# Kernel optimization log

Hardware: AMD Instinct MI355X
Metric: run time of the kernel (lower is better)

## Reference

```python
import jax, jax.numpy as jnp
import numpy as np

B, S, D, H = 8, 4096, 256, 256
MEM_COUNT = 3
FEAT = 7 * D + 2


def setup_inputs() -> dict:
    key = jax.random.key(0)
    ks = jax.random.split(key, 12)
    u = lambda k, shp: jax.random.uniform(k, shp, jnp.float32, -0.05, 0.05)
    return {
        "c": jax.random.normal(ks[0], (B, S, D), jnp.float32),
        "q": jax.random.normal(ks[1], (B, 1, D), jnp.float32),
        "len_c": jax.random.randint(ks[2], (B,), 1, S + 1),
        "att_weight": u(ks[3], (D, D)),
        "w1": u(ks[4], (H, FEAT)),
        "b1": jnp.zeros((H,), jnp.float32),
        "w2": u(ks[5], (1, H)),
        "b2": jnp.zeros((1,), jnp.float32),
        "w_ih": u(ks[6], (3 * D, D)),
        "w_hh": u(ks[7], (3 * D, D)),
        "b_ih": jnp.zeros((3 * D,), jnp.float32),
        "b_hh": jnp.zeros((3 * D,), jnp.float32),
    }


def gru_cell(x, h, w_ih, w_hh, b_ih, b_hh):
    # PyTorch GRUCell math
    gi = x @ w_ih.T + b_ih
    gh = h @ w_hh.T + b_hh
    i_r, i_z, i_n = jnp.split(gi, 3, axis=-1)
    h_r, h_z, h_n = jnp.split(gh, 3, axis=-1)
    r = jax.nn.sigmoid(i_r + h_r)
    z = jax.nn.sigmoid(i_z + h_z)
    n = jnp.tanh(i_n + r * h_n)
    return (1.0 - z) * n + z * h


def reference(c, q, len_c, att_weight, w1, b1, w2, b2, w_ih, w_hh, b_ih, b_hh):
    Bv, Sv, Dv = c.shape
    mask = jnp.arange(Sv)[None, :] < len_c[:, None]  # [B,S] valid positions
    cw = c @ att_weight                              # [B,S,D], reused each hop
    dot_q = jnp.einsum("bsd,bod->bso", cw, q)        # [B,S,1]
    m = q                                            # [B,1,D]
    atts = []
    for _ in range(MEM_COUNT):
        dot_m = jnp.einsum("bsd,bod->bso", cw, m)
        mb = jnp.broadcast_to(m, c.shape)
        qb = jnp.broadcast_to(q, c.shape)
        feat = jnp.concatenate(
            [c, mb, qb, c * q, c * m, jnp.abs(c - q), jnp.abs(c - m), dot_q, dot_m],
            axis=2,
        )                                            # [B,S,7D+2]
        h = jnp.tanh(feat @ w1.T + b1)               # [B,S,H]
        scores = (h @ w2.T + b2)[..., 0]             # [B,S]
        scores = jnp.where(mask, scores, -jnp.inf)
        att = jax.nn.softmax(scores, axis=1)
        att = jnp.where(mask, att, 0.0)[..., None]   # padded positions -> 0
        atts.append(att)
        e = (c * att).sum(axis=1)                    # [B,D]
        h_new = gru_cell(e, m[:, 0, :], w_ih, w_hh, b_ih, b_hh)
        m = h_new[:, None, :]
    return m[:, 0, :], jnp.stack(atts)
```

## Files before the change

kernel.cpp:

```cpp
#include <hip/hip_runtime.h>
#include <hip/hip_bf16.h>
#include <math.h>
#include <stdint.h>

#define B 8
#define S 4096
#define D 256
#define H 256
#define FEAT 1794
#define R (B*S)
#define DH (D*H)
#define NCH 64

typedef __bf16 bf16_t;
typedef __bf16 bf16x8 __attribute__((ext_vector_type(8)));
typedef float f32x4 __attribute__((ext_vector_type(4)));

__device__ __forceinline__ float waveReduceSum(float v) {
  #pragma unroll
  for (int off = 32; off; off >>= 1) v += __shfl_xor(v, off, 64);
  return v;
}

__global__ void k_init(const float* __restrict__ c, const float* __restrict__ q,
                       const float* __restrict__ w1, const float* __restrict__ A,
                       const int* __restrict__ len_c,
                       bf16_t* __restrict__ CBF, bf16_t* __restrict__ WAQ,
                       bf16_t* __restrict__ WAM, float* __restrict__ vq,
                       float* __restrict__ m0) {
  const int PREC_BLKS = R*D/2048;
  const int W_BLKS = DH/256;
  const int blk = blockIdx.x;
  if (blk < PREC_BLKS) {
    const int row0 = blk * 8;
    const int b = row0 >> 12;
    if ((row0 & 4095) >= len_c[b]) return;
    int gid = blk * 256 + threadIdx.x;
    const float* cp = c + (size_t)gid*8;
    float cv[8];
    *(float4*)(cv)   = *(const float4*)(cp);
    *(float4*)(cv+4) = *(const float4*)(cp + 4);
    bf16x8 cb;
    #pragma unroll
    for (int i = 0; i < 8; i++) cb[i] = (bf16_t)cv[i];
    *(bf16x8*)(CBF + (size_t)gid*8) = cb;
  } else if (blk < PREC_BLKS + W_BLKS) {
    int idx = (blk - PREC_BLKS) * 256 + threadIdx.x;
    int h = idx >> 8, k = idx & 255;
    const float* w1h = w1 + (size_t)h * FEAT;
    WAQ[idx] = (bf16_t)w1h[5*D + k];
    WAM[idx] = (bf16_t)w1h[6*D + k];
  } else {
    const int blk2 = blk - PREC_BLKS - W_BLKS;
    const int b = blk2 >> 6;
    const int lane = threadIdx.x & 63, wave = threadIdx.x >> 6;
    const int t = (blk2 & 63)*4 + wave;
    const int l4 = lane * 4;
    float4 q4 = *(const float4*)(q + b*D + l4);
    float4 a4 = *(const float4*)(A + (size_t)t*D + l4);
    float s = a4.x*q4.x + a4.y*q4.y + a4.z*q4.z + a4.w*q4.w;
    s = waveReduceSum(s);
    if (lane == 0) vq[b*D + t] = s;
    if (threadIdx.x < 4) {
      const int tt = (blk2 & 63)*4 + threadIdx.x;
      m0[b*D + tt] = q[b*D + tt];
    }
  }
}


__global__ void k_pm2(const float* __restrict__ A, const float* __restrict__ w1,
                      const float* __restrict__ b1, const float* __restrict__ q,
                      const float* __restrict__ min_,
                      float* __restrict__ vm, float* __restrict__ hb) {
  const int blk = blockIdx.x;
  const int b = blk >> 6;
  const int lane = threadIdx.x & 63, wave = threadIdx.x >> 6;
  const int t = (blk & 63)*4 + wave;
  const int l4 = lane * 4;
  float4 m4 = *(const float4*)(min_ + b*D + l4);
  float4 q4 = *(const float4*)(q + b*D + l4);
  float4 a4 = *(const float4*)(A + (size_t)t*D + l4);
  const float* w1r = w1 + (size_t)t*FEAT;
  float2 wm0 = *(const float2*)(w1r + D + l4);
  float2 wm1 = *(const float2*)(w1r + D + l4 + 2);
  float2 wq0 = *(const float2*)(w1r + 2*D + l4);
  float2 wq1 = *(const float2*)(w1r + 2*D + l4 + 2);
  float sv = a4.x*m4.x + a4.y*m4.y + a4.z*m4.z + a4.w*m4.w;
  float sh = m4.x*wm0.x + m4.y*wm0.y + m4.z*wm1.x + m4.w*wm1.y
           + q4.x*wq0.x + q4.y*wq0.y + q4.z*wq1.x + q4.w*wq1.y;
  sv = waveReduceSum(sv);
  sh = waveReduceSum(sh);
  if (lane == 0) { vm[b*D + t] = sv; hb[b*H + t] = b1[t] + sh; }
}

__global__ void k_comb(const float* __restrict__ w1, const float* __restrict__ q,
                       const float* __restrict__ min_,
                       const float* __restrict__ vq, const float* __restrict__ vm,
                       bf16_t* __restrict__ WCB) {
  int idx = blockIdx.x * 256 + threadIdx.x;
  int b = idx >> 16;
  int h = (idx >> 8) & 255;
  int k = idx & 255;
  const float* w1h = w1 + (size_t)h * FEAT;
  float v = w1h[k] + q[b*D + k]*w1h[3*D + k] + min_[b*D + k]*w1h[4*D + k]
          + vq[b*D + k]*w1h[7*D] + vm[b*D + k]*w1h[7*D + 1];
  WCB[idx] = (bf16_t)v;
}

__global__ __launch_bounds__(512, 4) void k_score6(
    const bf16_t* __restrict__ CBF,
    const bf16_t* __restrict__ WCB, const bf16_t* __restrict__ WAQ,
    const bf16_t* __restrict__ WAM,
    const float* __restrict__ q, const float* __restrict__ min_,
    const int* __restrict__ len_c,
    const float* __restrict__ hb, const float* __restrict__ w2,
    const float* __restrict__ b2, float* __restrict__ scores) {
  __shared__ char smem[49152];
  __shared__ float qshf[256], mshf[256];
  __shared__ float red[8][64];
  const int t = threadIdx.x;
  const int lane = t & 63, wave = t >> 6;
  const int r0 = blockIdx.x * 64;
  const int b = r0 >> 12;
  if ((r0 & 4095) >= len_c[b]) return;
  const int lrow = lane & 15;
  const int lk = (lane >> 4) * 8;
  const int n0 = wave * 32;

  if (t < 256) { qshf[t] = q[b*D + t]; mshf[t] = min_[b*D + t]; }

  const int srow = t >> 3, sl = t & 7;
  const int sp = sl ^ (srow & 7);
  const int swbase = srow*128 + sp*16;
  const bf16_t* cgp = CBF + (size_t)(r0 + srow)*D + sl*8;

  const bf16_t* bptrC = WCB + (size_t)b*DH;
  const bf16_t* bptrQ = WAQ;
  const bf16_t* bptrM = WAM;

  f32x4 acc[4][2];
  #pragma unroll
  for (int mi = 0; mi < 4; mi++)
    #pragma unroll
    for (int ni = 0; ni < 2; ni++) acc[mi][ni] = (f32x4){0.f,0.f,0.f,0.f};

  bf16x8 breg[2][6];
  #define LOADB(ks) { \
    const int kelem = (ks)*32 + lk; \
    _Pragma("unroll") \
    for (int ni = 0; ni < 2; ni++) { \
      const size_t co = (size_t)(n0 + ni*16 + lrow) * D + kelem; \
      breg[(ks)&1][ni*3+0] = *(const bf16x8*)(bptrC + co); \
      breg[(ks)&1][ni*3+1] = *(const bf16x8*)(bptrQ + co); \
      breg[(ks)&1][ni*3+2] = *(const bf16x8*)(bptrM + co); \
    } }

  #define STAGESC(mc, cc, cr) { \
    const int kof = (mc)*128 + (cc)*64 + sl*8; \
    float qv_[8], mv_[8]; \
    *(float4*)(qv_)   = *(const float4*)(qshf + kof); \
    *(float4*)(qv_+4) = *(const float4*)(qshf + kof + 4); \
    *(float4*)(mv_)   = *(const float4*)(mshf + kof); \
    *(float4*)(mv_+4) = *(const float4*)(mshf + kof + 4); \
    bf16x8 aqv_, amv_; \
    _Pragma("unroll") \
    for (int i = 0; i < 8; i++) { \
      float cf_ = (float)(cr)[i]; \
      aqv_[i] = (bf16_t)fabsf(cf_ - qv_[i]); \
      amv_[i] = (bf16_t)fabsf(cf_ - mv_[i]); \
    } \
    char* lb_ = smem + (cc)*8192 + swbase; \
    *(bf16x8*)(lb_)         = (cr); \
    *(bf16x8*)(lb_ + 16384) = aqv_; \
    *(bf16x8*)(lb_ + 32768) = amv_; \
  }

  bf16x8 cA = *(const bf16x8*)(cgp);
  bf16x8 cB = *(const bf16x8*)(cgp + 64);
  LOADB(0);
  __syncthreads();
  STAGESC(0, 0, cA);
  STAGESC(0, 1, cB);
  cA = *(const bf16x8*)(cgp + 128);
  cB = *(const bf16x8*)(cgp + 192);
  __syncthreads();

  #pragma unroll
  for (int ks = 0; ks < 4; ks++) {
    LOADB(ks + 1);
    const int cc = ks >> 1, kk = ks & 1;
    const int p = ((kk << 2) + (lane >> 4)) ^ (lane & 7);
    const char* lb = smem + cc*8192;
    #pragma unroll
    for (int mi = 0; mi < 4; mi++) {
      const int ro = (mi*16 + lrow)*128 + p*16;
      bf16x8 ac = *(const bf16x8*)(lb + ro);
      bf16x8 aq = *(const bf16x8*)(lb + 16384 + ro);
      bf16x8 am = *(const bf16x8*)(lb + 32768 + ro);
      #pragma unroll
      for (int ni = 0; ni < 2; ni++) {
        acc[mi][ni] = __builtin_amdgcn_mfma_f32_16x16x32_bf16(ac, breg[ks&1][ni*3+0], acc[mi][ni], 0, 0, 0);
        acc[mi][ni] = __builtin_amdgcn_mfma_f32_16x16x32_bf16(aq, breg[ks&1][ni*3+1], acc[mi][ni], 0, 0, 0);
        acc[mi][ni] = __builtin_amdgcn_mfma_f32_16x16x32_bf16(am, breg[ks&1][ni*3+2], acc[mi][ni], 0, 0, 0);
      }
    }
  }
  __syncthreads();
  STAGESC(1, 0, cA);
  STAGESC(1, 1, cB);
  __syncthreads();

  #pragma unroll
  for (int ks = 4; ks < 8; ks++) {
    if (ks < 7) LOADB(ks + 1);
    const int cc = (ks >> 1) & 1, kk = ks & 1;
    const int p = ((kk << 2) + (lane >> 4)) ^ (lane & 7);
    const char* lb = smem + cc*8192;
    #pragma unroll
    for (int mi = 0; mi < 4; mi++) {
      const int ro = (mi*16 + lrow)*128 + p*16;
      bf16x8 ac = *(const bf16x8*)(lb + ro);
      bf16x8 aq = *(const bf16x8*)(lb + 16384 + ro);
      bf16x8 am = *(const bf16x8*)(lb + 32768 + ro);
      #pragma unroll
      for (int ni = 0; ni < 2; ni++) {
        acc[mi][ni] = __builtin_amdgcn_mfma_f32_16x16x32_bf16(ac, breg[ks&1][ni*3+0], acc[mi][ni], 0, 0, 0);
        acc[mi][ni] = __builtin_amdgcn_mfma_f32_16x16x32_bf16(aq, breg[ks&1][ni*3+1], acc[mi][ni], 0, 0, 0);
        acc[mi][ni] = __builtin_amdgcn_mfma_f32_16x16x32_bf16(am, breg[ks&1][ni*3+2], acc[mi][ni], 0, 0, 0);
      }
    }
  }

  float hbv[2], w2v[2];
  #pragma unroll
  for (int ni = 0; ni < 2; ni++) {
    const int col = n0 + ni*16 + lrow;
    hbv[ni] = hb[b*H + col];
    w2v[ni] = w2[col];
  }
  #pragma unroll
  for (int mi = 0; mi < 4; mi++) {
    #pragma unroll
    for (int j = 0; j < 4; j++) {
      float ps = 0.f;
      #pragma unroll
      for (int ni = 0; ni < 2; ni++) {
        float x = acc[mi][ni][j] + hbv[ni];
        float ex = __expf(2.f * x);
        float th = 1.f - 2.f * __builtin_amdgcn_rcpf(ex + 1.f);
        ps += th * w2v[ni];
      }
      ps += __shfl_xor(ps, 1, 64);
      ps += __shfl_xor(ps, 2, 64);
      ps += __shfl_xor(ps, 4, 64);
      ps += __shfl_xor(ps, 8, 64);
      if (lrow == 0) red[wave][mi*16 + (lane >> 4)*4 + j] = ps;
    }
  }
  __syncthreads();
  if (t < 64) {
    float s = red[0][t] + red[1][t] + red[2][t] + red[3][t]
            + red[4][t] + red[5][t] + red[6][t] + red[7][t] + b2[0];
    scores[r0 + t] = s;
  }
}

__global__ __launch_bounds__(1024) void k_soft(const float* __restrict__ scores,
                                               const int* __restrict__ len_c,
                                               float* __restrict__ att) {
  const int b = blockIdx.x, t = threadIdx.x;
  const int len = len_c[b];
  __shared__ float rbuf[16];
  const float* sc = scores + b*S;
  float mx = -1e30f;
  for (int s = t; s < len; s += 1024) mx = fmaxf(mx, sc[s]);
  #pragma unroll
  for (int off = 32; off; off >>= 1) mx = fmaxf(mx, __shfl_xor(mx, off, 64));
  if ((t & 63) == 0) rbuf[t >> 6] = mx;
  __syncthreads();
  mx = rbuf[0];
  #pragma unroll
  for (int i = 1; i < 16; i++) mx = fmaxf(mx, rbuf[i]);
  __syncthreads();
  float sum = 0.f;
  float* ab = att + b*S;
  for (int s = t; s < S; s += 1024) {
    if (s < len) { float e = __expf(sc[s] - mx); ab[s] = e; sum += e; }
    else ab[s] = 0.f;
  }
  sum = waveReduceSum(sum);
  if ((t & 63) == 0) rbuf[t >> 6] = sum;
  __syncthreads();
  sum = 0.f;
  #pragma unroll
  for (int i = 0; i < 16; i++) sum += rbuf[i];
  const float inv = 1.f / sum;
  for (int s = t; s < len; s += 1024) ab[s] *= inv;
}

__global__ __launch_bounds__(256) void k_epart3(
    const bf16_t* __restrict__ CBF, const float* __restrict__ att,
    const int* __restrict__ len_c, float* __restrict__ epart) {
  const int b = blockIdx.x >> 6, ch = blockIdx.x & 63;
  const int t = threadIdx.x;
  const int s0 = ch * 64;
  if (s0 >= len_c[b]) {
    epart[(ch*B + b)*D + t] = 0.f;
    return;
  }
  __shared__ float esh[64];
  __shared__ float racc[8][256];
  if (t < 64) esh[t] = att[b*S + s0 + t];
  __syncthreads();
  const int cg = t & 31, rg = t >> 5;
  float a8[8];
  #pragma unroll
  for (int i = 0; i < 8; i++) a8[i] = 0.f;
  #pragma unroll
  for (int j = 0; j < 8; j++) {
    const int srow = rg + j*8;
    const bf16x8 cv = *(const bf16x8*)(CBF + (size_t)(b*S + s0 + srow)*D + cg*8);
    const float a = esh[srow];
    #pragma unroll
    for (int i = 0; i < 8; i++) a8[i] += a * (float)cv[i];
  }
  *(float4*)(&racc[rg][cg*8])     = *(float4*)(a8);
  *(float4*)(&racc[rg][cg*8 + 4]) = *(float4*)(a8 + 4);
  __syncthreads();
  float s = 0.f;
  #pragma unroll
  for (int g = 0; g < 8; g++) s += racc[g][t];
  epart[(ch*B + b)*D + t] = s;
}

__global__ __launch_bounds__(256) void k_gru2(
    const float* __restrict__ wih, const float* __restrict__ whh,
    const float* __restrict__ bih, const float* __restrict__ bhh,
    const float* __restrict__ epart, const float* __restrict__ min_,
    float* __restrict__ mout, float* __restrict__ out, const int write_out) {
  const int blk = blockIdx.x;
  const int b = blk >> 4;
  const int t0 = (blk & 15) << 4;
  const int t = threadIdx.x;
  const int lane = t & 63, wave = t >> 6;
  __shared__ float es[D], ms[D];
  float e = 0.f;
  #pragma unroll
  for (int ch = 0; ch < NCH; ch++) e += epart[(ch*B + b)*D + t];
  es[t] = e;
  ms[t] = min_[b*D + t];
  __syncthreads();
  const int l4 = lane * 4;
  float4 e4 = *(const float4*)(es + l4);
  float4 m4 = *(const float4*)(ms + l4);
  #pragma unroll
  for (int tl = 0; tl < 4; tl++) {
    const int tt = t0 + wave*4 + tl;
    float g[6];
    #pragma unroll
    for (int gg = 0; gg < 3; gg++) {
      const int j = gg*D + tt;
      const float4 wi4 = *(const float4*)(wih + (size_t)j*D + l4);
      const float4 wh4 = *(const float4*)(whh + (size_t)j*D + l4);
      float gi = e4.x*wi4.x + e4.y*wi4.y + e4.z*wi4.z + e4.w*wi4.w;
      float gh = m4.x*wh4.x + m4.y*wh4.y + m4.z*wh4.z + m4.w*wh4.w;
      g[gg]   = waveReduceSum(gi);
      g[3+gg] = waveReduceSum(gh);
    }
    if (lane == 0) {
      const int j0 = tt, j1 = D + tt, j2 = 2*D + tt;
      float gir = g[0] + bih[j0], giz = g[1] + bih[j1], gin = g[2] + bih[j2];
      float ghr = g[3] + bhh[j0], ghz = g[4] + bhh[j1], ghn = g[5] + bhh[j2];
      float rr = 1.f / (1.f + __expf(-(gir + ghr)));
      float zz = 1.f / (1.f + __expf(-(giz + ghz)));
      float nn = tanhf(gin + rr * ghn);
      float mn = (1.f - zz)*nn + zz*ms[tt];
      mout[b*D + tt] = mn;
      if (write_out) out[b*D + tt] = mn;
    }
  }
}

extern "C" void kernel_launch(void* const* d_in, const int* in_sizes, int n_in,
                              void* d_out, int out_size, void* d_ws, size_t ws_size,
                              hipStream_t stream) {
  const float* c   = (const float*)d_in[0];
  const float* q   = (const float*)d_in[1];
  const int*   len = (const int*)d_in[2];
  const float* A   = (const float*)d_in[3];
  const float* w1  = (const float*)d_in[4];
  const float* b1  = (const float*)d_in[5];
  const float* w2  = (const float*)d_in[6];
  const float* b2  = (const float*)d_in[7];
  const float* wih = (const float*)d_in[8];
  const float* whh = (const float*)d_in[9];
  const float* bih = (const float*)d_in[10];
  const float* bhh = (const float*)d_in[11];
  float* out = (float*)d_out;

  bf16_t* WCB = (bf16_t*)d_ws;
  bf16_t* WAQ = WCB + (size_t)B*DH;
  bf16_t* WAM = WAQ + DH;
  bf16_t* CBF = WAM + DH;
  float* fb = (float*)(CBF + (size_t)R*D);
  float* vq    = fb;
  float* vm    = vq + B*D;
  float* hb    = vm + B*D;
  float* m0    = hb + B*H;
  float* m1    = m0 + B*D;
  float* epart = m1 + B*D;
  float* sc    = epart + (size_t)NCH*B*D;

  k_init<<<R*D/2048 + DH/256 + B*64, 256, 0, stream>>>(c, q, w1, A, len, CBF, WAQ, WAM, vq, m0);

  for (int it = 0; it < 3; ++it) {
    float* min_ = (it & 1) ? m1 : m0;
    float* mout = (it & 1) ? m0 : m1;
    k_pm2<<<B*64, 256, 0, stream>>>(A, w1, b1, q, min_, vm, hb);
    k_comb<<<B*DH/256, 256, 0, stream>>>(w1, q, min_, vq, vm, WCB);
    k_score6<<<R/64, 512, 0, stream>>>(CBF, WCB, WAQ, WAM, q, min_, len, hb, w2, b2, sc);
    float* att = out + B*D + (size_t)it*R;
    k_soft<<<B, 1024, 0, stream>>>(sc, len, att);
    k_epart3<<<B*NCH, 256, 0, stream>>>(CBF, att, len, epart);
    k_gru2<<<B*16, 256, 0, stream>>>(wih, whh, bih, bhh, epart, min_, mout, out, it == 2 ? 1 : 0);
  }
}
```

Baseline: 156.4 us.

## Fold softmax into score, epart and GRU kernels; compact score grid over valid rows

```diff
diff --git a/kernel.cpp b/kernel.cpp
--- a/kernel.cpp
+++ b/kernel.cpp
@@ -108,22 +108,31 @@
   WCB[idx] = (bf16_t)v;
 }
 
-__global__ __launch_bounds__(512, 4) void k_score6(
+__global__ __launch_bounds__(512, 4) void k_score7(
     const bf16_t* __restrict__ CBF,
     const bf16_t* __restrict__ WCB, const bf16_t* __restrict__ WAQ,
     const bf16_t* __restrict__ WAM,
     const float* __restrict__ q, const float* __restrict__ min_,
     const int* __restrict__ len_c,
     const float* __restrict__ hb, const float* __restrict__ w2,
-    const float* __restrict__ b2, float* __restrict__ scores) {
+    const float* __restrict__ b2, float* __restrict__ esc) {
+  int b = 0, r0l = -1, accb = 0;
+  const int flat = blockIdx.x;
+  #pragma unroll
+  for (int bb = 0; bb < 8; bb++) {
+    const int nb = (len_c[bb] + 63) >> 6;
+    if (r0l < 0 && flat < accb + nb) { b = bb; r0l = (flat - accb) << 6; }
+    accb += nb;
+  }
+  if (r0l < 0) return;
+  const int len = len_c[b];
+  const int rowg = b*S + r0l;
+
   __shared__ char smem[49152];
   __shared__ float qshf[256], mshf[256];
   __shared__ float red[8][64];
   const int t = threadIdx.x;
   const int lane = t & 63, wave = t >> 6;
-  const int r0 = blockIdx.x * 64;
-  const int b = r0 >> 12;
-  if ((r0 & 4095) >= len_c[b]) return;
   const int lrow = lane & 15;
   const int lk = (lane >> 4) * 8;
   const int n0 = wave * 32;
@@ -133,7 +142,7 @@
   const int srow = t >> 3, sl = t & 7;
   const int sp = sl ^ (srow & 7);
   const int swbase = srow*128 + sp*16;
-  const bf16_t* cgp = CBF + (size_t)(r0 + srow)*D + sl*8;
+  const bf16_t* cgp = CBF + (size_t)(rowg + srow)*D + sl*8;
 
   const bf16_t* bptrC = WCB + (size_t)b*DH;
   const bf16_t* bptrQ = WAQ;
@@ -262,57 +271,30 @@
   if (t < 64) {
     float s = red[0][t] + red[1][t] + red[2][t] + red[3][t]
             + red[4][t] + red[5][t] + red[6][t] + red[7][t] + b2[0];
-    scores[r0 + t] = s;
-  }
-}
-
-__global__ __launch_bounds__(1024) void k_soft(const float* __restrict__ scores,
-                                               const int* __restrict__ len_c,
-                                               float* __restrict__ att) {
-  const int b = blockIdx.x, t = threadIdx.x;
-  const int len = len_c[b];
-  __shared__ float rbuf[16];
-  const float* sc = scores + b*S;
-  float mx = -1e30f;
-  for (int s = t; s < len; s += 1024) mx = fmaxf(mx, sc[s]);
-  #pragma unroll
-  for (int off = 32; off; off >>= 1) mx = fmaxf(mx, __shfl_xor(mx, off, 64));
-  if ((t & 63) == 0) rbuf[t >> 6] = mx;
-  __syncthreads();
-  mx = rbuf[0];
-  #pragma unroll
-  for (int i = 1; i < 16; i++) mx = fmaxf(mx, rbuf[i]);
-  __syncthreads();
-  float sum = 0.f;
-  float* ab = att + b*S;
-  for (int s = t; s < S; s += 1024) {
-    if (s < len) { float e = __expf(sc[s] - mx); ab[s] = e; sum += e; }
-    else ab[s] = 0.f;
-  }
-  sum = waveReduceSum(sum);
-  if ((t & 63) == 0) rbuf[t >> 6] = sum;
-  __syncthreads();
-  sum = 0.f;
-  #pragma unroll
-  for (int i = 0; i < 16; i++) sum += rbuf[i];
-  const float inv = 1.f / sum;
-  for (int s = t; s < len; s += 1024) ab[s] *= inv;
-}
-
-__global__ __launch_bounds__(256) void k_epart3(
-    const bf16_t* __restrict__ CBF, const float* __restrict__ att,
-    const int* __restrict__ len_c, float* __restrict__ epart) {
+    esc[b*S + r0l + t] = (r0l + t < len) ? __expf(s) : 0.f;
+  }
+}
+
+__global__ __launch_bounds__(256) void k_epart4(
+    const bf16_t* __restrict__ CBF, const float* __restrict__ esc,
+    const int* __restrict__ len_c, float* __restrict__ epart,
+    float* __restrict__ ssum) {
   const int b = blockIdx.x >> 6, ch = blockIdx.x & 63;
   const int t = threadIdx.x;
   const int s0 = ch * 64;
   if (s0 >= len_c[b]) {
     epart[(ch*B + b)*D + t] = 0.f;
+    if (t == 0) ssum[ch*B + b] = 0.f;
     return;
   }
   __shared__ float esh[64];
   __shared__ float racc[8][256];
-  if (t < 64) esh[t] = att[b*S + s0 + t];
-  __syncthreads();
+  if (t < 64) esh[t] = esc[b*S + s0 + t];
+  __syncthreads();
+  if (t < 64) {
+    float v = waveReduceSum(esh[t]);
+    if (t == 0) ssum[ch*B + b] = v;
+  }
   const int cg = t & 31, rg = t >> 5;
   float a8[8];
   #pragma unroll
@@ -334,23 +316,37 @@
   epart[(ch*B + b)*D + t] = s;
 }
 
-__global__ __launch_bounds__(256) void k_gru2(
+__global__ __launch_bounds__(256) void k_gru3(
     const float* __restrict__ wih, const float* __restrict__ whh,
     const float* __restrict__ bih, const float* __restrict__ bhh,
-    const float* __restrict__ epart, const float* __restrict__ min_,
-    float* __restrict__ mout, float* __restrict__ out, const int write_out) {
+    const float* __restrict__ epart, const float* __restrict__ ssum,
+    const float* __restrict__ esc, const int* __restrict__ len_c,
+    const float* __restrict__ min_,
+    float* __restrict__ att, float* __restrict__ mout,
+    float* __restrict__ out, const int write_out) {
   const int blk = blockIdx.x;
   const int b = blk >> 4;
-  const int t0 = (blk & 15) << 4;
+  const int p = blk & 15;
   const int t = threadIdx.x;
   const int lane = t & 63, wave = t >> 6;
+  const int len = len_c[b];
   __shared__ float es[D], ms[D];
+  __shared__ float Tsh;
+  if (t < 64) {
+    float v = waveReduceSum(ssum[t*B + b]);
+    if (t == 0) Tsh = v;
+  }
   float e = 0.f;
   #pragma unroll
   for (int ch = 0; ch < NCH; ch++) e += epart[(ch*B + b)*D + t];
-  es[t] = e;
   ms[t] = min_[b*D + t];
   __syncthreads();
+  const float Tinv = 1.f / Tsh;
+  es[t] = e * Tinv;
+  const int sI = p*256 + t;
+  att[b*S + sI] = (sI < len) ? esc[b*S + sI] * Tinv : 0.f;
+  __syncthreads();
+  const int t0 = p << 4;
   const int l4 = lane * 4;
   float4 e4 = *(const float4*)(es + l4);
   float4 m4 = *(const float4*)(ms + l4);
@@ -410,7 +406,8 @@
   float* m0    = hb + B*H;
   float* m1    = m0 + B*D;
   float* epart = m1 + B*D;
-  float* sc    = epart + (size_t)NCH*B*D;
+  float* esc   = epart + (size_t)NCH*B*D;
+  float* ssum  = esc + R;
 
   k_init<<<R*D/2048 + DH/256 + B*64, 256, 0, stream>>>(c, q, w1, A, len, CBF, WAQ, WAM, vq, m0);
 
@@ -419,10 +416,9 @@
     float* mout = (it & 1) ? m0 : m1;
     k_pm2<<<B*64, 256, 0, stream>>>(A, w1, b1, q, min_, vm, hb);
     k_comb<<<B*DH/256, 256, 0, stream>>>(w1, q, min_, vq, vm, WCB);
-    k_score6<<<R/64, 512, 0, stream>>>(CBF, WCB, WAQ, WAM, q, min_, len, hb, w2, b2, sc);
+    k_score7<<<R/64, 512, 0, stream>>>(CBF, WCB, WAQ, WAM, q, min_, len, hb, w2, b2, esc);
     float* att = out + B*D + (size_t)it*R;
-    k_soft<<<B, 1024, 0, stream>>>(sc, len, att);
-    k_epart3<<<B*NCH, 256, 0, stream>>>(CBF, att, len, epart);
-    k_gru2<<<B*16, 256, 0, stream>>>(wih, whh, bih, bhh, epart, min_, mout, out, it == 2 ? 1 : 0);
-  }
-}
+    k_epart4<<<B*NCH, 256, 0, stream>>>(CBF, esc, len, epart, ssum);
+    k_gru3<<<B*16, 256, 0, stream>>>(wih, whh, bih, bhh, epart, ssum, esc, len, min_, att, mout, out, it == 2 ? 1 : 0);
+  }
+}
```

Result: faster. 147.0 us (-6.0%).
